# Performance work log

Measured on AMD Instinct MI355X. Metric: run time of the kernel, lower is better.

## Reference

```python
import jax, jax.numpy as jnp
import numpy as np

N_NODES = 50000
N_EDGES = 800000
IN_F, EDGE_F, HID, HEADS, OUT_F = 128, 16, 32, 4, 128
NEG_SLOPE = 0.2


def edge_gat_layer(h, ef, src, dst, W, We, al, ar, ae, b, act):
    """One DGL-style EdgeGATConv layer.
    h: [N, Fin], ef: [E, Fe], W: [Fin, H*D], We: [Fe, H*D],
    al/ar/ae: [H, D], b: [H*D]. Returns [N, H*D].
    """
    N = h.shape[0]
    H, D = al.shape
    feat = (h @ W).reshape(N, H, D)                    # [N,H,D]
    fe = (ef @ We).reshape(-1, H, D)                   # [E,H,D]
    el = jnp.einsum('nhd,hd->nh', feat, al)            # [N,H]
    er = jnp.einsum('nhd,hd->nh', feat, ar)            # [N,H]
    ee = jnp.einsum('ehd,hd->eh', fe, ae)              # [E,H]
    e = jax.nn.leaky_relu(el[src] + er[dst] + ee, NEG_SLOPE)  # [E,H]
    # edge softmax over incoming edges of each dst node
    emax = jax.ops.segment_max(e, dst, num_segments=N)        # [N,H]
    ex = jnp.exp(e - emax[dst])                               # [E,H]
    esum = jax.ops.segment_sum(ex, dst, num_segments=N)       # [N,H]
    a = ex / esum[dst]                                        # [E,H]
    msg = feat[src] * a[:, :, None]                           # [E,H,D]
    rst = jax.ops.segment_sum(msg, dst, num_segments=N)       # [N,H,D]
    rst = rst + b.reshape(1, H, D)
    if act:
        rst = jax.nn.relu(rst)
    return rst.reshape(N, H * D)


def _glorot(k, shape):
    fan = shape[0]
    return jax.random.normal(k, shape, dtype=jnp.float32) / np.sqrt(fan)


def setup_inputs() -> dict:
    key = jax.random.key(0)
    ks = jax.random.split(key, 24)
    inp = {
        'h': jax.random.normal(ks[0], (N_NODES, IN_F), dtype=jnp.float32),
        'edge_feats': jax.random.normal(ks[1], (N_EDGES, EDGE_F), dtype=jnp.float32),
        'src': jax.random.randint(ks[2], (N_EDGES,), 0, N_NODES, dtype=jnp.int32),
        'dst': jax.random.randint(ks[3], (N_EDGES,), 0, N_NODES, dtype=jnp.int32),
    }
    # layer 0: IN_F -> HEADS*HID ; layer 1: HEADS*HID -> HEADS*HID ; layer 2: heads=1, OUT_F
    dims = [(IN_F, HEADS, HID), (HEADS * HID, HEADS, HID), (HEADS * HID, 1, OUT_F)]
    ki = 4
    for i, (fin, H, D) in enumerate(dims):
        inp[f'W{i}'] = _glorot(ks[ki], (fin, H * D)); ki += 1
        inp[f'We{i}'] = _glorot(ks[ki], (EDGE_F, H * D)); ki += 1
        inp[f'al{i}'] = _glorot(ks[ki], (H, D)); ki += 1
        inp[f'ar{i}'] = _glorot(ks[ki], (H, D)); ki += 1
        inp[f'ae{i}'] = _glorot(ks[ki], (H, D)); ki += 1
        inp[f'b{i}'] = jnp.zeros((H * D,), dtype=jnp.float32)
    return inp


def reference(h, edge_feats, src, dst,
              W0, We0, al0, ar0, ae0, b0,
              W1, We1, al1, ar1, ae1, b1,
              W2, We2, al2, ar2, ae2, b2):
    h = edge_gat_layer(h, edge_feats, src, dst, W0, We0, al0, ar0, ae0, b0, True)
    h = edge_gat_layer(h, edge_feats, src, dst, W1, We1, al1, ar1, ae1, b1, True)
    h = edge_gat_layer(h, edge_feats, src, dst, W2, We2, al2, ar2, ae2, b2, False)
    return h
```

## Files before the change

kernel.cpp:

```cpp
#include <hip/hip_runtime.h>
#include <hip/hip_fp16.h>
#include <cstdint>

#define NN 50000
#define NE 800000
static constexpr int HD = 128;
static constexpr int EF_DIM = 16;
static constexpr int SCAN_B = 256;
static constexpr int NPARTS = (NN + SCAN_B - 1) / SCAN_B;
static constexpr int EBLK = (NE + 255) / 256;
static constexpr int FG = (NN + 63) / 64;

typedef _Float16 f16x4 __attribute__((ext_vector_type(4)));
typedef float f32x4 __attribute__((ext_vector_type(4)));

struct RecP {
    int src;
    int e;
    f16x4 p0;
    f16x4 p1;
    _Float16 p2;
    _Float16 pad;
};
union Rec32 { RecP r; float4 v[2]; };


__global__ void k_zero(int* __restrict__ cnt) {
    int i = blockIdx.x * blockDim.x + threadIdx.x;
    if (i < NN) cnt[i] = 0;
}

__global__ __launch_bounds__(256) void k_prep2(const float* __restrict__ h,
        const int* __restrict__ dst,
        const float* __restrict__ We0, const float* __restrict__ ae0,
        const float* __restrict__ We1, const float* __restrict__ ae1,
        const float* __restrict__ We2, const float* __restrict__ ae2,
        const float* __restrict__ W0, const float* __restrict__ W1,
        const float* __restrict__ W2,
        int* __restrict__ cnt, int* __restrict__ pos_loc, float* __restrict__ M,
        _Float16* __restrict__ Wht, _Float16* __restrict__ Xh) {
    int b = blockIdx.x;
    const int t = threadIdx.x;
    if (b < EBLK) {
        int e = b * 256 + t;
        if (e < NE) pos_loc[e] = atomicAdd(&cnt[dst[e]], 1);
        return;
    }
    b -= EBLK;
    if (b < 3) {
        int l = b;
        const float* We = (l == 0) ? We0 : (l == 1) ? We1 : We2;
        const float* ae = (l == 0) ? ae0 : (l == 1) ? ae1 : ae2;
        int H = (l == 2) ? 1 : 4, D = (l == 2) ? 128 : 32;
        if (t < EF_DIM * H) {
            int f = t / H, hh = t % H;
            float s = 0.f;
            for (int d = 0; d < D; d++) s += We[f * HD + hh * D + d] * ae[hh * D + d];
            M[l * 64 + f * H + hh] = s;
        }
        return;
    }
    if (b < 195) {
        int i = (b - 3) * 256 + t;
        int l = i >> 14, rem = i & 16383;
        int n = rem >> 7, k = rem & 127;
        const float* W = (l == 0) ? W0 : (l == 1) ? W1 : W2;
        Wht[(size_t)l * 16384 + n * 128 + k] = (_Float16)W[k * 128 + n];
        return;
    }
    {
        int i = (b - 195) * 256 + t;
        if (i < NN * 32) {
            float4 v = ((const float4*)h)[i];
            f16x4 o = {(_Float16)v.x, (_Float16)v.y, (_Float16)v.z, (_Float16)v.w};
            ((f16x4*)Xh)[i] = o;
        }
    }
}

__global__ __launch_bounds__(SCAN_B) void k_part(const int* __restrict__ deg,
                                                 int* __restrict__ part) {
    __shared__ int s[SCAN_B];
    int t = threadIdx.x;
    int i = blockIdx.x * SCAN_B + t;
    s[t] = (i < NN) ? deg[i] : 0;
    __syncthreads();
    for (int off = SCAN_B / 2; off > 0; off >>= 1) {
        if (t < off) s[t] += s[t + off];
        __syncthreads();
    }
    if (t == 0) part[blockIdx.x] = s[0];
}

__global__ __launch_bounds__(SCAN_B) void k_scanpart(int* __restrict__ part) {
    __shared__ int s[SCAN_B];
    int t = threadIdx.x;
    int v = (t < NPARTS) ? part[t] : 0;
    s[t] = v;
    __syncthreads();
    for (int off = 1; off < SCAN_B; off <<= 1) {
        int u = (t >= off) ? s[t - off] : 0;
        __syncthreads();
        s[t] += u;
        __syncthreads();
    }
    if (t < NPARTS) part[t] = s[t] - v;
}

__global__ __launch_bounds__(SCAN_B) void k_rowptr(const int* __restrict__ deg,
                                                   const int* __restrict__ part,
                                                   int* __restrict__ row_ptr) {
    __shared__ int s[SCAN_B];
    int t = threadIdx.x;
    int i = blockIdx.x * SCAN_B + t;
    int v = (i < NN) ? deg[i] : 0;
    s[t] = v;
    __syncthreads();
    for (int off = 1; off < SCAN_B; off <<= 1) {
        int u = (t >= off) ? s[t - off] : 0;
        __syncthreads();
        s[t] += u;
        __syncthreads();
    }
    int excl = s[t] - v + part[blockIdx.x];
    if (i < NN) row_ptr[i] = excl;
    if (i == NN) row_ptr[NN] = NE;
}

__global__ __launch_bounds__(256) void k_place(const int* __restrict__ src,
                                               const int* __restrict__ dst,
                                               const int* __restrict__ pos_loc,
                                               const float* __restrict__ EFt,
                                               const float* __restrict__ M,
                                               const int* __restrict__ row_ptr,
                                               float4* __restrict__ rec) {
    __shared__ float sM[192];
    int t = threadIdx.x;
    if (t < 192) sM[t] = M[t];
    __syncthreads();
    int e = blockIdx.x * 256 + t;
    if (e >= NE) return;
    float ef[EF_DIM];
    const float4* efp = (const float4*)(EFt + (size_t)e * EF_DIM);
#pragma unroll
    for (int q = 0; q < 4; q++) {
        float4 v = efp[q];
        ef[4 * q] = v.x; ef[4 * q + 1] = v.y; ef[4 * q + 2] = v.z; ef[4 * q + 3] = v.w;
    }
    float o0[4] = {0.f, 0.f, 0.f, 0.f};
    float o1[4] = {0.f, 0.f, 0.f, 0.f};
    float o2 = 0.f;
#pragma unroll
    for (int f = 0; f < EF_DIM; f++) {
        float v = ef[f];
#pragma unroll
        for (int hh = 0; hh < 4; hh++) {
            o0[hh] += v * sM[f * 4 + hh];
            o1[hh] += v * sM[64 + f * 4 + hh];
        }
        o2 += v * sM[128 + f];
    }
    Rec32 u;
    u.r.src = src[e];
    u.r.e = e;
    u.r.p0 = f16x4{(_Float16)o0[0], (_Float16)o0[1], (_Float16)o0[2], (_Float16)o0[3]};
    u.r.p1 = f16x4{(_Float16)o1[0], (_Float16)o1[1], (_Float16)o1[2], (_Float16)o1[3]};
    u.r.p2 = (_Float16)o2;
    u.r.pad = (_Float16)0.f;
    int pos = row_ptr[dst[e]] + pos_loc[e];
    rec[(size_t)pos * 2] = u.v[0];
    rec[(size_t)pos * 2 + 1] = u.v[1];
}

__global__ __launch_bounds__(256) void k_segsort2(const int* __restrict__ row_ptr,
                                                  const float4* __restrict__ rec,
                                                  int* __restrict__ ssrc,
                                                  f16x4* __restrict__ ep0,
                                                  f16x4* __restrict__ ep1,
                                                  _Float16* __restrict__ ep2) {
    __shared__ Rec32 seg[4][128];
    const int wave = threadIdx.x >> 6;
    const int lane = threadIdx.x & 63;
    const int n = blockIdx.x * 4 + wave;
    const int start = row_ptr[n];
    const int len = row_ptr[n + 1] - start;
    const bool small = (len > 0 && len <= 128);
    if (small)
        for (int s = lane; s < len; s += 64) {
            seg[wave][s].v[0] = rec[(size_t)(start + s) * 2];
            seg[wave][s].v[1] = rec[(size_t)(start + s) * 2 + 1];
        }
    __syncthreads();
    if (small) {
        for (int s = lane; s < len; s += 64) {
            RecP me = seg[wave][s].r;
            int rank = 0;
            for (int j = 0; j < len; j++) {
                const RecP& o = seg[wave][j].r;
                rank += (o.src < me.src) || (o.src == me.src && o.e < me.e);
            }
            int w = start + rank;
            ssrc[w] = me.src;
            ep0[w] = me.p0;
            ep1[w] = me.p1;
            ep2[w] = me.p2;
        }
    } else if (len > 128) {
        for (int s = lane; s < len; s += 64) {
            Rec32 u;
            u.v[0] = rec[(size_t)(start + s) * 2];
            u.v[1] = rec[(size_t)(start + s) * 2 + 1];
            int w = start + s;
            ssrc[w] = u.r.src;
            ep0[w] = u.r.p0;
            ep1[w] = u.r.p1;
            ep2[w] = u.r.p2;
        }
    }
}

template <int H>
__global__ __launch_bounds__(256) void k_feat(const _Float16* __restrict__ Xh,
                                              const _Float16* __restrict__ Wht,
                                              const float* __restrict__ al,
                                              const float* __restrict__ ar,
                                              _Float16* __restrict__ Fh,
                                              float* __restrict__ el,
                                              float* __restrict__ er) {
    const int t = threadIdx.x;
    const int lane = t & 63;
    const int wv = t >> 6;
    const int l15 = lane & 15;
    const int kg = lane >> 4;
    const int nbase = blockIdx.x * 64;
    const int arow = nbase + wv * 16 + l15;
    const int rclamp = (arow < NN) ? arow : NN - 1;
    const int ksub = kg * 4;
    f16x4 a[8];
#pragma unroll
    for (int kb = 0; kb < 8; kb++)
        a[kb] = *(const f16x4*)(Xh + (size_t)rclamp * 128 + kb * 16 + ksub);

    const int r0 = nbase + wv * 16 + kg * 4;
    float slp[4][H], srp[4][H];
#pragma unroll
    for (int r = 0; r < 4; r++)
#pragma unroll
        for (int hh = 0; hh < H; hh++) { slp[r][hh] = 0.f; srp[r][hh] = 0.f; }

#pragma unroll
    for (int nt = 0; nt < 8; nt++) {
        f32x4 acc = {0.f, 0.f, 0.f, 0.f};
        const int nc = nt * 16 + l15;
        const _Float16* wp = Wht + (size_t)nc * 128;
#pragma unroll
        for (int kb = 0; kb < 8; kb++) {
            f16x4 bf = *(const f16x4*)(wp + kb * 16 + ksub);
            acc = __builtin_amdgcn_mfma_f32_16x16x16f16(a[kb], bf, acc, 0, 0, 0);
        }
        const float alv = al[nc], arv = ar[nc];
        const int hsel = (H == 4) ? (nt >> 1) : 0;
#pragma unroll
        for (int r = 0; r < 4; r++) {
            int ro = r0 + r;
            if (ro < NN) Fh[(size_t)ro * 128 + nc] = (_Float16)acc[r];
            slp[r][hsel] += acc[r] * alv;
            srp[r][hsel] += acc[r] * arv;
        }
    }

#pragma unroll
    for (int m = 1; m < 16; m <<= 1)
#pragma unroll
        for (int r = 0; r < 4; r++)
#pragma unroll
            for (int hh = 0; hh < H; hh++) {
                slp[r][hh] += __shfl_xor(slp[r][hh], m);
                srp[r][hh] += __shfl_xor(srp[r][hh], m);
            }

    if (H == 4) {
        int r = l15 >> 2, hh2 = l15 & 3;
        float sv = 0.f, ev = 0.f;
#pragma unroll
        for (int rr = 0; rr < 4; rr++)
#pragma unroll
            for (int hc = 0; hc < H; hc++)
                if (rr == r && hc == hh2) { sv = slp[rr][hc]; ev = srp[rr][hc]; }
        int ro = r0 + r;
        if (ro < NN) { el[ro * 4 + hh2] = sv; er[ro * 4 + hh2] = ev; }
    } else {
        if (l15 < 4) {
            float sv = 0.f, ev = 0.f;
#pragma unroll
            for (int rr = 0; rr < 4; rr++)
                if (rr == l15) { sv = slp[rr][0]; ev = srp[rr][0]; }
            int ro = r0 + l15;
            if (ro < NN) { el[ro] = sv; er[ro] = ev; }
        }
    }
}

template <int H, int D, int OUT16>
__global__ __launch_bounds__(256) void k_node(const int* __restrict__ row_ptr,
                                              const int* __restrict__ ssrc,
                                              const _Float16* __restrict__ ep,
                                              const float* __restrict__ el,
                                              const float* __restrict__ er,
                                              const __half2* __restrict__ Fh,
                                              const float* __restrict__ bias,
                                              float* __restrict__ Rf,
                                              _Float16* __restrict__ Rh,
                                              int act) {
    __shared__ float wlds[4][256];
    const int wave = threadIdx.x >> 6;
    const int lane = threadIdx.x & 63;
    const int n = blockIdx.x * 4 + wave;
    const int start = row_ptr[n];
    const int end = row_ptr[n + 1];
    const int len = end - start;
    const int slots = len * H;
    const int c = 2 * lane;
    const int hcol = c / D;
    float2 b2 = make_float2(bias[c], bias[c + 1]);
    float2 a = make_float2(0.f, 0.f);

    if (len > 0) {
        constexpr int hsh = (H == 4) ? 2 : 0;
        const int hh = lane & (H - 1);
        const float er_j = er[n * H + hh];
        const _Float16* epb = ep + (size_t)start * H;
        float pmax = -3.0e38f, psum = 0.f;

        if (slots <= 256) {
            float* wp = wlds[wave];
            for (int jj = lane; jj < slots; jj += 64) {
                int i = start + (jj >> hsh);
                float x = el[ssrc[i] * H + hh] + er_j + (float)epb[jj];
                x = (x > 0.f) ? x : 0.2f * x;
                wp[jj] = x;
                pmax = fmaxf(pmax, x);
            }
            for (int m = H; m < 64; m <<= 1) pmax = fmaxf(pmax, __shfl_xor(pmax, m));
            for (int jj = lane; jj < slots; jj += 64) {
                float ex = __expf(wp[jj] - pmax);
                wp[jj] = ex;
                psum += ex;
            }
            for (int m = H; m < 64; m <<= 1) psum += __shfl_xor(psum, m);
            const float inv = 1.f / __shfl(psum, hcol);
#pragma unroll 4
            for (int i = start; i < end; i++) {
                float w = wp[(i - start) * H + hcol];
                float2 f2 = __half22float2(Fh[(size_t)ssrc[i] * 64 + lane]);
                a.x += f2.x * w;
                a.y += f2.y * w;
            }
            a.x *= inv;
            a.y *= inv;
        } else {
            for (int jj = lane; jj < slots; jj += 64) {
                int i = start + (jj >> hsh);
                float x = el[ssrc[i] * H + hh] + er_j + (float)epb[jj];
                x = (x > 0.f) ? x : 0.2f * x;
                pmax = fmaxf(pmax, x);
            }
            for (int m = H; m < 64; m <<= 1) pmax = fmaxf(pmax, __shfl_xor(pmax, m));
            for (int jj = lane; jj < slots; jj += 64) {
                int i = start + (jj >> hsh);
                float x = el[ssrc[i] * H + hh] + er_j + (float)epb[jj];
                x = (x > 0.f) ? x : 0.2f * x;
                psum += __expf(x - pmax);
            }
            for (int m = H; m < 64; m <<= 1) psum += __shfl_xor(psum, m);
            const float inv = 1.f / __shfl(psum, hcol);
            const float pm_c = __shfl(pmax, hcol);
            const float er_c = er[n * H + hcol];
            for (int i = start; i < end; i++) {
                int sn = ssrc[i];
                float x = el[sn * H + hcol] + er_c + (float)epb[(i - start) * H + hcol];
                x = (x > 0.f) ? x : 0.2f * x;
                float w = __expf(x - pm_c);
                float2 f2 = __half22float2(Fh[(size_t)sn * 64 + lane]);
                a.x += f2.x * w;
                a.y += f2.y * w;
            }
            a.x *= inv;
            a.y *= inv;
        }
    }

    float2 v = make_float2(a.x + b2.x, a.y + b2.y);
    if (act) { v.x = fmaxf(v.x, 0.f); v.y = fmaxf(v.y, 0.f); }
    if (OUT16)
        ((__half2*)Rh)[(size_t)n * 64 + lane] = __floats2half2_rn(v.x, v.y);
    else
        ((float2*)Rf)[(size_t)n * 64 + lane] = v;
}


extern "C" void kernel_launch(void* const* d_in, const int* in_sizes, int n_in,
                              void* d_out, int out_size, void* d_ws, size_t ws_size,
                              hipStream_t stream) {
    const float* h   = (const float*)d_in[0];
    const float* eft = (const float*)d_in[1];
    const int* src   = (const int*)d_in[2];
    const int* dst   = (const int*)d_in[3];
    auto P = [&](int i) { return (const float*)d_in[i]; };

    float* ws = (float*)d_ws;
    float4* rec    = (float4*)ws;
    _Float16* Fh   = (_Float16*)ws;
    float* el      = ws + 3200000;
    float* er      = ws + 3400000;
    _Float16* Xh   = (_Float16*)(ws + 6400000);
    _Float16* Wht  = Xh + (size_t)NN * 128;
    _Float16* ep0s = Wht + 3 * 16384;
    _Float16* ep1s = ep0s + (size_t)NE * 4;
    _Float16* ep2s = ep1s + (size_t)NE * 4;
    int* ssrc      = (int*)(ep2s + NE);
    int* pos_loc   = ssrc + NE;
    float* M       = (float*)(pos_loc + NE);
    int* row_ptr   = (int*)(M + 192);
    int* cnt       = row_ptr + (NN + 1);
    int* part      = cnt + NN;
    float* out     = (float*)d_out;

    hipLaunchKernelGGL(k_zero, dim3(NPARTS), dim3(256), 0, stream, cnt);
    hipLaunchKernelGGL(k_prep2, dim3(EBLK + 195 + (NN * 32 + 255) / 256), dim3(256), 0,
                       stream, h, dst, P(5), P(8), P(11), P(14), P(17), P(20),
                       P(4), P(10), P(16), cnt, pos_loc, M, Wht, Xh);
    hipLaunchKernelGGL(k_part, dim3(NPARTS), dim3(SCAN_B), 0, stream, cnt, part);
    hipLaunchKernelGGL(k_scanpart, dim3(1), dim3(SCAN_B), 0, stream, part);
    hipLaunchKernelGGL(k_rowptr, dim3(NPARTS), dim3(SCAN_B), 0, stream,
                       cnt, part, row_ptr);
    hipLaunchKernelGGL(k_place, dim3(EBLK), dim3(256), 0, stream,
                       src, dst, pos_loc, eft, M, row_ptr, rec);
    hipLaunchKernelGGL(k_segsort2, dim3(NN / 4), dim3(256), 0, stream,
                       row_ptr, rec, ssrc, (f16x4*)ep0s, (f16x4*)ep1s, ep2s);

    hipLaunchKernelGGL((k_feat<4>), dim3(FG), dim3(256), 0, stream,
                       Xh, Wht, P(6), P(7), Fh, el, er);
    hipLaunchKernelGGL((k_node<4, 32, 1>), dim3(NN / 4), dim3(256), 0, stream,
                       row_ptr, ssrc, ep0s, el, er, (const __half2*)Fh, P(9),
                       nullptr, Xh, 1);
    hipLaunchKernelGGL((k_feat<4>), dim3(FG), dim3(256), 0, stream,
                       Xh, Wht + 16384, P(12), P(13), Fh, el, er);
    hipLaunchKernelGGL((k_node<4, 32, 1>), dim3(NN / 4), dim3(256), 0, stream,
                       row_ptr, ssrc, ep1s, el, er, (const __half2*)Fh, P(15),
                       nullptr, Xh, 1);
    hipLaunchKernelGGL((k_feat<1>), dim3(FG), dim3(256), 0, stream,
                       Xh, Wht + 32768, P(18), P(19), Fh, el, er);
    hipLaunchKernelGGL((k_node<1, 128, 0>), dim3(NN / 4), dim3(256), 0, stream,
                       row_ptr, ssrc, ep2s, el, er, (const __half2*)Fh, P(21),
                       out, nullptr, 0);
}
```

Baseline: 366.0 us.

## Fuse next-layer feature transform and attention logits into node aggregation kernel

The aggregation kernel for layers 0 and 1 now also applies bias and ReLU, then multiplies the node's output row by the next layer's fp16 weight matrix. It writes the next layer's half-precision features plus el/er logits directly, which removes two separate k_feat launches and the round trip through the intermediate activation buffer. The GEMV runs on scalar FMA, reading every weight row from global memory per wave, where k_feat presumably used tiled matrix ops. That adds per-node compute and weight traffic in exchange for fewer launches and less memory traffic. Buffers are ping-ponged (FhA/FhB aliasing Xh) so each fused kernel does not overwrite its own inputs.

```diff
diff --git a/kernel.cpp b/kernel.cpp
--- a/kernel.cpp
+++ b/kernel.cpp
@@ -10,6 +10,7 @@
 static constexpr int NPARTS = (NN + SCAN_B - 1) / SCAN_B;
 static constexpr int EBLK = (NE + 255) / 256;
 static constexpr int FG = (NN + 63) / 64;
+static constexpr int XH_BLK = (NN * 32 + 255) / 256;
 
 typedef _Float16 f16x4 __attribute__((ext_vector_type(4)));
 typedef float f32x4 __attribute__((ext_vector_type(4)));
@@ -38,7 +39,8 @@
         const float* __restrict__ W0, const float* __restrict__ W1,
         const float* __restrict__ W2,
         int* __restrict__ cnt, int* __restrict__ pos_loc, float* __restrict__ M,
-        _Float16* __restrict__ Wht, _Float16* __restrict__ Xh) {
+        _Float16* __restrict__ Wht, _Float16* __restrict__ Xh,
+        _Float16* __restrict__ Whn1, _Float16* __restrict__ Whn2) {
     int b = blockIdx.x;
     const int t = threadIdx.x;
     if (b < EBLK) {
@@ -68,13 +70,20 @@
         Wht[(size_t)l * 16384 + n * 128 + k] = (_Float16)W[k * 128 + n];
         return;
     }
-    {
+    if (b < 195 + XH_BLK) {
         int i = (b - 195) * 256 + t;
         if (i < NN * 32) {
             float4 v = ((const float4*)h)[i];
             f16x4 o = {(_Float16)v.x, (_Float16)v.y, (_Float16)v.z, (_Float16)v.w};
             ((f16x4*)Xh)[i] = o;
         }
+        return;
+    }
+    {
+        int i = (b - 195 - XH_BLK) * 256 + t;
+        int l = i >> 14, rem = i & 16383;
+        if (l == 0) Whn1[rem] = (_Float16)W1[rem];
+        else        Whn2[rem] = (_Float16)W2[rem];
     }
 }
 
@@ -301,7 +310,139 @@
     }
 }
 
-template <int H, int D, int OUT16>
+template <int H, int D, int HN>
+__global__ __launch_bounds__(256) void k_node_feat(const int* __restrict__ row_ptr,
+                                                   const int* __restrict__ ssrc,
+                                                   const _Float16* __restrict__ ep,
+                                                   const float* __restrict__ el,
+                                                   const float* __restrict__ er,
+                                                   const __half2* __restrict__ Fh,
+                                                   const float* __restrict__ bias,
+                                                   const _Float16* __restrict__ Whn,
+                                                   const float* __restrict__ aln,
+                                                   const float* __restrict__ arn,
+                                                   __half2* __restrict__ Fh_next,
+                                                   float* __restrict__ el_next,
+                                                   float* __restrict__ er_next) {
+    __shared__ float wlds[4][256];
+    __shared__ float vbuf[4][128];
+    const int wave = threadIdx.x >> 6;
+    const int lane = threadIdx.x & 63;
+    const int n = blockIdx.x * 4 + wave;
+    const int start = row_ptr[n];
+    const int end = row_ptr[n + 1];
+    const int len = end - start;
+    const int slots = len * H;
+    const int c = 2 * lane;
+    const int hcol = c / D;
+    float2 b2 = make_float2(bias[c], bias[c + 1]);
+    float2 a = make_float2(0.f, 0.f);
+
+    if (len > 0) {
+        constexpr int hsh = (H == 4) ? 2 : 0;
+        const int hh = lane & (H - 1);
+        const float er_j = er[n * H + hh];
+        const _Float16* epb = ep + (size_t)start * H;
+        float pmax = -3.0e38f, psum = 0.f;
+
+        if (slots <= 256) {
+            float* wp = wlds[wave];
+            for (int jj = lane; jj < slots; jj += 64) {
+                int i = start + (jj >> hsh);
+                float x = el[ssrc[i] * H + hh] + er_j + (float)epb[jj];
+                x = (x > 0.f) ? x : 0.2f * x;
+                wp[jj] = x;
+                pmax = fmaxf(pmax, x);
+            }
+            for (int m = H; m < 64; m <<= 1) pmax = fmaxf(pmax, __shfl_xor(pmax, m));
+            for (int jj = lane; jj < slots; jj += 64) {
+                float ex = __expf(wp[jj] - pmax);
+                wp[jj] = ex;
+                psum += ex;
+            }
+            for (int m = H; m < 64; m <<= 1) psum += __shfl_xor(psum, m);
+            const float inv = 1.f / __shfl(psum, hcol);
+#pragma unroll 4
+            for (int i = start; i < end; i++) {
+                float w = wp[(i - start) * H + hcol];
+                float2 f2 = __half22float2(Fh[(size_t)ssrc[i] * 64 + lane]);
+                a.x += f2.x * w;
+                a.y += f2.y * w;
+            }
+            a.x *= inv;
+            a.y *= inv;
+        } else {
+            for (int jj = lane; jj < slots; jj += 64) {
+                int i = start + (jj >> hsh);
+                float x = el[ssrc[i] * H + hh] + er_j + (float)epb[jj];
+                x = (x > 0.f) ? x : 0.2f * x;
+                pmax = fmaxf(pmax, x);
+            }
+            for (int m = H; m < 64; m <<= 1) pmax = fmaxf(pmax, __shfl_xor(pmax, m));
+            for (int jj = lane; jj < slots; jj += 64) {
+                int i = start + (jj >> hsh);
+                float x = el[ssrc[i] * H + hh] + er_j + (float)epb[jj];
+                x = (x > 0.f) ? x : 0.2f * x;
+                psum += __expf(x - pmax);
+            }
+            for (int m = H; m < 64; m <<= 1) psum += __shfl_xor(psum, m);
+            const float inv = 1.f / __shfl(psum, hcol);
+            const float pm_c = __shfl(pmax, hcol);
+            const float er_c = er[n * H + hcol];
+            for (int i = start; i < end; i++) {
+                int sn = ssrc[i];
+                float x = el[sn * H + hcol] + er_c + (float)epb[(i - start) * H + hcol];
+                x = (x > 0.f) ? x : 0.2f * x;
+                float w = __expf(x - pm_c);
+                float2 f2 = __half22float2(Fh[(size_t)sn * 64 + lane]);
+                a.x += f2.x * w;
+                a.y += f2.y * w;
+            }
+            a.x *= inv;
+            a.y *= inv;
+        }
+    }
+
+    float2 v = make_float2(fmaxf(a.x + b2.x, 0.f), fmaxf(a.y + b2.y, 0.f));
+    vbuf[wave][c] = v.x;
+    vbuf[wave][c + 1] = v.y;
+
+    float2 acc2 = make_float2(0.f, 0.f);
+#pragma unroll 4
+    for (int k = 0; k < 128; k++) {
+        float vk = vbuf[wave][k];
+        float2 wv = __half22float2(((const __half2*)(Whn + (size_t)k * 128))[lane]);
+        acc2.x += vk * wv.x;
+        acc2.y += vk * wv.y;
+    }
+    Fh_next[(size_t)n * 64 + lane] = __floats2half2_rn(acc2.x, acc2.y);
+
+    float sl = acc2.x * aln[c] + acc2.y * aln[c + 1];
+    float sr = acc2.x * arn[c] + acc2.y * arn[c + 1];
+    if (HN == 4) {
+#pragma unroll
+        for (int m = 1; m < 16; m <<= 1) {
+            sl += __shfl_xor(sl, m);
+            sr += __shfl_xor(sr, m);
+        }
+        if ((lane & 15) == 0) {
+            el_next[n * 4 + (lane >> 4)] = sl;
+            er_next[n * 4 + (lane >> 4)] = sr;
+        }
+    } else {
+#pragma unroll
+        for (int m = 1; m < 64; m <<= 1) {
+            sl += __shfl_xor(sl, m);
+            sr += __shfl_xor(sr, m);
+        }
+        if (lane == 0) {
+            el_next[n] = sl;
+            er_next[n] = sr;
+        }
+    }
+}
+
+template <int H, int D>
 __global__ __launch_bounds__(256) void k_node(const int* __restrict__ row_ptr,
                                               const int* __restrict__ ssrc,
                                               const _Float16* __restrict__ ep,
@@ -309,9 +450,7 @@
                                               const float* __restrict__ er,
                                               const __half2* __restrict__ Fh,
                                               const float* __restrict__ bias,
-                                              float* __restrict__ Rf,
-                                              _Float16* __restrict__ Rh,
-                                              int act) {
+                                              float* __restrict__ Rf) {
     __shared__ float wlds[4][256];
     const int wave = threadIdx.x >> 6;
     const int lane = threadIdx.x & 63;
@@ -391,11 +530,7 @@
     }
 
     float2 v = make_float2(a.x + b2.x, a.y + b2.y);
-    if (act) { v.x = fmaxf(v.x, 0.f); v.y = fmaxf(v.y, 0.f); }
-    if (OUT16)
-        ((__half2*)Rh)[(size_t)n * 64 + lane] = __floats2half2_rn(v.x, v.y);
-    else
-        ((float2*)Rf)[(size_t)n * 64 + lane] = v;
+    ((float2*)Rf)[(size_t)n * 64 + lane] = v;
 }
 
 
@@ -410,9 +545,11 @@
 
     float* ws = (float*)d_ws;
     float4* rec    = (float4*)ws;
-    _Float16* Fh   = (_Float16*)ws;
-    float* el      = ws + 3200000;
-    float* er      = ws + 3400000;
+    _Float16* FhA  = (_Float16*)ws;
+    float* elA     = ws + 3200000;
+    float* erA     = ws + 3400000;
+    float* elC     = ws + 3600000;
+    float* erC     = ws + 3700000;
     _Float16* Xh   = (_Float16*)(ws + 6400000);
     _Float16* Wht  = Xh + (size_t)NN * 128;
     _Float16* ep0s = Wht + 3 * 16384;
@@ -424,12 +561,18 @@
     int* row_ptr   = (int*)(M + 192);
     int* cnt       = row_ptr + (NN + 1);
     int* part      = cnt + NN;
+    float* elB     = (float*)(part + NPARTS + 64);
+    float* erB     = elB + (size_t)NN * 4;
+    _Float16* Whn1 = (_Float16*)(erB + (size_t)NN * 4);
+    _Float16* Whn2 = Whn1 + 16384;
+    _Float16* FhB  = Xh;
+    _Float16* FhC  = FhA;
     float* out     = (float*)d_out;
 
     hipLaunchKernelGGL(k_zero, dim3(NPARTS), dim3(256), 0, stream, cnt);
-    hipLaunchKernelGGL(k_prep2, dim3(EBLK + 195 + (NN * 32 + 255) / 256), dim3(256), 0,
+    hipLaunchKernelGGL(k_prep2, dim3(EBLK + 195 + XH_BLK + 128), dim3(256), 0,
                        stream, h, dst, P(5), P(8), P(11), P(14), P(17), P(20),
-                       P(4), P(10), P(16), cnt, pos_loc, M, Wht, Xh);
+                       P(4), P(10), P(16), cnt, pos_loc, M, Wht, Xh, Whn1, Whn2);
     hipLaunchKernelGGL(k_part, dim3(NPARTS), dim3(SCAN_B), 0, stream, cnt, part);
     hipLaunchKernelGGL(k_scanpart, dim3(1), dim3(SCAN_B), 0, stream, part);
     hipLaunchKernelGGL(k_rowptr, dim3(NPARTS), dim3(SCAN_B), 0, stream,
@@ -440,18 +583,14 @@
                        row_ptr, rec, ssrc, (f16x4*)ep0s, (f16x4*)ep1s, ep2s);
 
     hipLaunchKernelGGL((k_feat<4>), dim3(FG), dim3(256), 0, stream,
-                       Xh, Wht, P(6), P(7), Fh, el, er);
-    hipLaunchKernelGGL((k_node<4, 32, 1>), dim3(NN / 4), dim3(256), 0, stream,
-                       row_ptr, ssrc, ep0s, el, er, (const __half2*)Fh, P(9),
-                       nullptr, Xh, 1);
-    hipLaunchKernelGGL((k_feat<4>), dim3(FG), dim3(256), 0, stream,
-                       Xh, Wht + 16384, P(12), P(13), Fh, el, er);
-    hipLaunchKernelGGL((k_node<4, 32, 1>), dim3(NN / 4), dim3(256), 0, stream,
-                       row_ptr, ssrc, ep1s, el, er, (const __half2*)Fh, P(15),
-                       nullptr, Xh, 1);
-    hipLaunchKernelGGL((k_feat<1>), dim3(FG), dim3(256), 0, stream,
-                       Xh, Wht + 32768, P(18), P(19), Fh, el, er);
-    hipLaunchKernelGGL((k_node<1, 128, 0>), dim3(NN / 4), dim3(256), 0, stream,
-                       row_ptr, ssrc, ep2s, el, er, (const __half2*)Fh, P(21),
-                       out, nullptr, 0);
-}
+                       Xh, Wht, P(6), P(7), FhA, elA, erA);
+    hipLaunchKernelGGL((k_node_feat<4, 32, 4>), dim3(NN / 4), dim3(256), 0, stream,
+                       row_ptr, ssrc, ep0s, elA, erA, (const __half2*)FhA, P(9),
+                       Whn1, P(12), P(13), (__half2*)FhB, elB, erB);
+    hipLaunchKernelGGL((k_node_feat<4, 32, 1>), dim3(NN / 4), dim3(256), 0, stream,
+                       row_ptr, ssrc, ep1s, elB, erB, (const __half2*)FhB, P(15),
+                       Whn2, P(18), P(19), (__half2*)FhC, elC, erC);
+    hipLaunchKernelGGL((k_node<1, 128>), dim3(NN / 4), dim3(256), 0, stream,
+                       row_ptr, ssrc, ep2s, elC, erC, (const __half2*)FhC, P(21),
+                       out);
+}
```

New measurement: 404.7 us. 10.6% more time.

## Compute edge records in edge order early and scatter only a permutation index

Applied to the files above, without the earlier changes.

The per-edge edge-feature projection moves out of the post-scan placement kernel into the big prep kernel, so records are written in original edge order and this work runs in parallel with the degree counting. The M projection moves into the zeroing kernel so it is ready beforehand. A small kernel then scatters just the edge id into CSR order, and the segment sort gathers records through that permutation. This shortens the serial chain after the scan and makes the scatter smaller, at the cost of an extra index array and random 32-byte gathers in the sort.

```diff
diff --git a/kernel.cpp b/kernel.cpp
--- a/kernel.cpp
+++ b/kernel.cpp
@@ -10,6 +10,7 @@
 static constexpr int NPARTS = (NN + SCAN_B - 1) / SCAN_B;
 static constexpr int EBLK = (NE + 255) / 256;
 static constexpr int FG = (NN + 63) / 64;
+static constexpr int XH_BLK = (NN * 32 + 255) / 256;
 
 typedef _Float16 f16x4 __attribute__((ext_vector_type(4)));
 typedef float f32x4 __attribute__((ext_vector_type(4)));
@@ -25,19 +26,36 @@
 union Rec32 { RecP r; float4 v[2]; };
 
 
-__global__ void k_zero(int* __restrict__ cnt) {
-    int i = blockIdx.x * blockDim.x + threadIdx.x;
-    if (i < NN) cnt[i] = 0;
-}
-
-__global__ __launch_bounds__(256) void k_prep2(const float* __restrict__ h,
-        const int* __restrict__ dst,
+__global__ __launch_bounds__(256) void k_zero(int* __restrict__ cnt,
         const float* __restrict__ We0, const float* __restrict__ ae0,
         const float* __restrict__ We1, const float* __restrict__ ae1,
         const float* __restrict__ We2, const float* __restrict__ ae2,
+        float* __restrict__ M) {
+    const int b = blockIdx.x, t = threadIdx.x;
+    if (b < NPARTS) {
+        int i = b * 256 + t;
+        if (i < NN) cnt[i] = 0;
+        return;
+    }
+    int l = b - NPARTS;
+    const float* We = (l == 0) ? We0 : (l == 1) ? We1 : We2;
+    const float* ae = (l == 0) ? ae0 : (l == 1) ? ae1 : ae2;
+    int H = (l == 2) ? 1 : 4, D = (l == 2) ? 128 : 32;
+    if (t < EF_DIM * H) {
+        int f = t / H, hh = t % H;
+        float s = 0.f;
+        for (int d = 0; d < D; d++) s += We[f * HD + hh * D + d] * ae[hh * D + d];
+        M[l * 64 + f * H + hh] = s;
+    }
+}
+
+__global__ __launch_bounds__(256) void k_prep3(const float* __restrict__ h,
+        const int* __restrict__ src, const int* __restrict__ dst,
+        const float* __restrict__ EFt, const float* __restrict__ M,
         const float* __restrict__ W0, const float* __restrict__ W1,
         const float* __restrict__ W2,
-        int* __restrict__ cnt, int* __restrict__ pos_loc, float* __restrict__ M,
+        int* __restrict__ cnt, int* __restrict__ pos_loc,
+        float4* __restrict__ rec,
         _Float16* __restrict__ Wht, _Float16* __restrict__ Xh) {
     int b = blockIdx.x;
     const int t = threadIdx.x;
@@ -47,21 +65,46 @@
         return;
     }
     b -= EBLK;
-    if (b < 3) {
-        int l = b;
-        const float* We = (l == 0) ? We0 : (l == 1) ? We1 : We2;
-        const float* ae = (l == 0) ? ae0 : (l == 1) ? ae1 : ae2;
-        int H = (l == 2) ? 1 : 4, D = (l == 2) ? 128 : 32;
-        if (t < EF_DIM * H) {
-            int f = t / H, hh = t % H;
-            float s = 0.f;
-            for (int d = 0; d < D; d++) s += We[f * HD + hh * D + d] * ae[hh * D + d];
-            M[l * 64 + f * H + hh] = s;
-        }
+    if (b < EBLK) {
+        __shared__ float sM[192];
+        if (t < 192) sM[t] = M[t];
+        __syncthreads();
+        int e = b * 256 + t;
+        if (e >= NE) return;
+        float ef[EF_DIM];
+        const float4* efp = (const float4*)(EFt + (size_t)e * EF_DIM);
+#pragma unroll
+        for (int q = 0; q < 4; q++) {
+            float4 v = efp[q];
+            ef[4 * q] = v.x; ef[4 * q + 1] = v.y; ef[4 * q + 2] = v.z; ef[4 * q + 3] = v.w;
+        }
+        float o0[4] = {0.f, 0.f, 0.f, 0.f};
+        float o1[4] = {0.f, 0.f, 0.f, 0.f};
+        float o2 = 0.f;
+#pragma unroll
+        for (int f = 0; f < EF_DIM; f++) {
+            float v = ef[f];
+#pragma unroll
+            for (int hh = 0; hh < 4; hh++) {
+                o0[hh] += v * sM[f * 4 + hh];
+                o1[hh] += v * sM[64 + f * 4 + hh];
+            }
+            o2 += v * sM[128 + f];
+        }
+        Rec32 u;
+        u.r.src = src[e];
+        u.r.e = e;
+        u.r.p0 = f16x4{(_Float16)o0[0], (_Float16)o0[1], (_Float16)o0[2], (_Float16)o0[3]};
+        u.r.p1 = f16x4{(_Float16)o1[0], (_Float16)o1[1], (_Float16)o1[2], (_Float16)o1[3]};
+        u.r.p2 = (_Float16)o2;
+        u.r.pad = (_Float16)0.f;
+        rec[(size_t)e * 2] = u.v[0];
+        rec[(size_t)e * 2 + 1] = u.v[1];
         return;
     }
-    if (b < 195) {
-        int i = (b - 3) * 256 + t;
+    b -= EBLK;
+    if (b < 192) {
+        int i = b * 256 + t;
         int l = i >> 14, rem = i & 16383;
         int n = rem >> 7, k = rem & 127;
         const float* W = (l == 0) ? W0 : (l == 1) ? W1 : W2;
@@ -69,7 +112,7 @@
         return;
     }
     {
-        int i = (b - 195) * 256 + t;
+        int i = (b - 192) * 256 + t;
         if (i < NN * 32) {
             float4 v = ((const float4*)h)[i];
             f16x4 o = {(_Float16)v.x, (_Float16)v.y, (_Float16)v.z, (_Float16)v.w};
@@ -127,52 +170,14 @@
     if (i == NN) row_ptr[NN] = NE;
 }
 
-__global__ __launch_bounds__(256) void k_place(const int* __restrict__ src,
-                                               const int* __restrict__ dst,
-                                               const int* __restrict__ pos_loc,
-                                               const float* __restrict__ EFt,
-                                               const float* __restrict__ M,
-                                               const int* __restrict__ row_ptr,
-                                               float4* __restrict__ rec) {
-    __shared__ float sM[192];
-    int t = threadIdx.x;
-    if (t < 192) sM[t] = M[t];
-    __syncthreads();
-    int e = blockIdx.x * 256 + t;
-    if (e >= NE) return;
-    float ef[EF_DIM];
-    const float4* efp = (const float4*)(EFt + (size_t)e * EF_DIM);
-#pragma unroll
-    for (int q = 0; q < 4; q++) {
-        float4 v = efp[q];
-        ef[4 * q] = v.x; ef[4 * q + 1] = v.y; ef[4 * q + 2] = v.z; ef[4 * q + 3] = v.w;
-    }
-    float o0[4] = {0.f, 0.f, 0.f, 0.f};
-    float o1[4] = {0.f, 0.f, 0.f, 0.f};
-    float o2 = 0.f;
-#pragma unroll
-    for (int f = 0; f < EF_DIM; f++) {
-        float v = ef[f];
-#pragma unroll
-        for (int hh = 0; hh < 4; hh++) {
-            o0[hh] += v * sM[f * 4 + hh];
-            o1[hh] += v * sM[64 + f * 4 + hh];
-        }
-        o2 += v * sM[128 + f];
-    }
-    Rec32 u;
-    u.r.src = src[e];
-    u.r.e = e;
-    u.r.p0 = f16x4{(_Float16)o0[0], (_Float16)o0[1], (_Float16)o0[2], (_Float16)o0[3]};
-    u.r.p1 = f16x4{(_Float16)o1[0], (_Float16)o1[1], (_Float16)o1[2], (_Float16)o1[3]};
-    u.r.p2 = (_Float16)o2;
-    u.r.pad = (_Float16)0.f;
-    int pos = row_ptr[dst[e]] + pos_loc[e];
-    rec[(size_t)pos * 2] = u.v[0];
-    rec[(size_t)pos * 2 + 1] = u.v[1];
-}
-
-__global__ __launch_bounds__(256) void k_segsort2(const int* __restrict__ row_ptr,
+__global__ void k_eperm(const int* __restrict__ dst, const int* __restrict__ pos_loc,
+                        const int* __restrict__ row_ptr, int* __restrict__ eperm) {
+    int e = blockIdx.x * blockDim.x + threadIdx.x;
+    if (e < NE) eperm[row_ptr[dst[e]] + pos_loc[e]] = e;
+}
+
+__global__ __launch_bounds__(256) void k_segsort3(const int* __restrict__ row_ptr,
+                                                  const int* __restrict__ eperm,
                                                   const float4* __restrict__ rec,
                                                   int* __restrict__ ssrc,
                                                   f16x4* __restrict__ ep0,
@@ -187,8 +192,9 @@
     const bool small = (len > 0 && len <= 128);
     if (small)
         for (int s = lane; s < len; s += 64) {
-            seg[wave][s].v[0] = rec[(size_t)(start + s) * 2];
-            seg[wave][s].v[1] = rec[(size_t)(start + s) * 2 + 1];
+            int e = eperm[start + s];
+            seg[wave][s].v[0] = rec[(size_t)e * 2];
+            seg[wave][s].v[1] = rec[(size_t)e * 2 + 1];
         }
     __syncthreads();
     if (small) {
@@ -207,9 +213,10 @@
         }
     } else if (len > 128) {
         for (int s = lane; s < len; s += 64) {
+            int e = eperm[start + s];
             Rec32 u;
-            u.v[0] = rec[(size_t)(start + s) * 2];
-            u.v[1] = rec[(size_t)(start + s) * 2 + 1];
+            u.v[0] = rec[(size_t)e * 2];
+            u.v[1] = rec[(size_t)e * 2 + 1];
             int w = start + s;
             ssrc[w] = u.r.src;
             ep0[w] = u.r.p0;
@@ -420,24 +427,26 @@
     _Float16* ep2s = ep1s + (size_t)NE * 4;
     int* ssrc      = (int*)(ep2s + NE);
     int* pos_loc   = ssrc + NE;
-    float* M       = (float*)(pos_loc + NE);
+    int* eperm     = pos_loc + NE;
+    float* M       = (float*)(eperm + NE);
     int* row_ptr   = (int*)(M + 192);
     int* cnt       = row_ptr + (NN + 1);
     int* part      = cnt + NN;
     float* out     = (float*)d_out;
 
-    hipLaunchKernelGGL(k_zero, dim3(NPARTS), dim3(256), 0, stream, cnt);
-    hipLaunchKernelGGL(k_prep2, dim3(EBLK + 195 + (NN * 32 + 255) / 256), dim3(256), 0,
-                       stream, h, dst, P(5), P(8), P(11), P(14), P(17), P(20),
-                       P(4), P(10), P(16), cnt, pos_loc, M, Wht, Xh);
+    hipLaunchKernelGGL(k_zero, dim3(NPARTS + 3), dim3(256), 0, stream, cnt,
+                       P(5), P(8), P(11), P(14), P(17), P(20), M);
+    hipLaunchKernelGGL(k_prep3, dim3(2 * EBLK + 192 + XH_BLK), dim3(256), 0, stream,
+                       h, src, dst, eft, M, P(4), P(10), P(16),
+                       cnt, pos_loc, rec, Wht, Xh);
     hipLaunchKernelGGL(k_part, dim3(NPARTS), dim3(SCAN_B), 0, stream, cnt, part);
     hipLaunchKernelGGL(k_scanpart, dim3(1), dim3(SCAN_B), 0, stream, part);
     hipLaunchKernelGGL(k_rowptr, dim3(NPARTS), dim3(SCAN_B), 0, stream,
                        cnt, part, row_ptr);
-    hipLaunchKernelGGL(k_place, dim3(EBLK), dim3(256), 0, stream,
-                       src, dst, pos_loc, eft, M, row_ptr, rec);
-    hipLaunchKernelGGL(k_segsort2, dim3(NN / 4), dim3(256), 0, stream,
-                       row_ptr, rec, ssrc, (f16x4*)ep0s, (f16x4*)ep1s, ep2s);
+    hipLaunchKernelGGL(k_eperm, dim3(EBLK), dim3(256), 0, stream,
+                       dst, pos_loc, row_ptr, eperm);
+    hipLaunchKernelGGL(k_segsort3, dim3(NN / 4), dim3(256), 0, stream,
+                       row_ptr, eperm, rec, ssrc, (f16x4*)ep0s, (f16x4*)ep1s, ep2s);
 
     hipLaunchKernelGGL((k_feat<4>), dim3(FG), dim3(256), 0, stream,
                        Xh, Wht, P(6), P(7), Fh, el, er);
```

Measured after the change: 373.0 us. Within noise of the previous version (+1.9%).
